# Kernel optimization log

Measured on AMD Instinct MI355X. Metric: run time of the kernel, lower is better.

The kernel has to match this reference:

```python
import jax, jax.numpy as jnp
import numpy as np

EMBED_DIM = 256
H = 80
W = 80
N_HEADS = 8
N_POINTS = 4
B = 8


def sine_pe(C, h, w):
    # LoFTR-style PositionEncodingSine, returns [1, C, h, w]
    y_pos = jnp.cumsum(jnp.ones((h, w), jnp.float32), axis=0)[None]
    x_pos = jnp.cumsum(jnp.ones((h, w), jnp.float32), axis=1)[None]
    div = jnp.exp(jnp.arange(0, C // 2, 2, dtype=jnp.float32) * (-np.log(10000.0) / (C // 2)))[:, None, None]
    pe = jnp.zeros((C, h, w), jnp.float32)
    pe = pe.at[0::4].set(jnp.sin(x_pos * div))
    pe = pe.at[1::4].set(jnp.cos(x_pos * div))
    pe = pe.at[2::4].set(jnp.sin(y_pos * div))
    pe = pe.at[3::4].set(jnp.cos(y_pos * div))
    return pe[None]


def make_reference_points(h, w):
    # Faithful to the original (W-major flatten, (col, row) stacking)
    gr = np.linspace(0, 1, w)
    gc = np.linspace(0, 1, h)
    R, Cg = np.meshgrid(gr, gc, indexing='ij')  # (w, h)
    ref = np.stack((Cg, R), -1).reshape(-1, 2)  # [w*h, 2]
    return jnp.asarray(ref, jnp.float32)


def setup_inputs():
    key = jax.random.key(0)
    ks = jax.random.split(key, 8)
    C = EMBED_DIM
    s = 1.0 / np.sqrt(C)
    return {
        'query': jax.random.normal(ks[0], (B, C, H, W), jnp.float32),
        'value': jax.random.normal(ks[1], (B, C, H, W), jnp.float32),
        'W_value': jax.random.normal(ks[2], (C, C), jnp.float32) * s,
        'b_value': jnp.zeros((C,), jnp.float32),
        'W_off': jax.random.normal(ks[3], (C, N_HEADS * N_POINTS * 2), jnp.float32) * 0.01,
        'b_off': jax.random.normal(ks[4], (N_HEADS * N_POINTS * 2,), jnp.float32) * 0.5,
        'W_attn': jax.random.normal(ks[5], (C, N_HEADS * N_POINTS), jnp.float32) * s,
        'b_attn': jnp.zeros((N_HEADS * N_POINTS,), jnp.float32),
        'W_out': jax.random.normal(ks[6], (C, C), jnp.float32) * s,
        'b_out': jnp.zeros((C,), jnp.float32),
    }


def _deform_attn_core(q, v, ref, W_off, b_off, W_attn, b_attn):
    # q: [B, Nq, C] queries; v: [B, H*W, C] projected values; ref: [Nq, 2]
    Bq, Nq, C = q.shape
    hd = C // N_HEADS
    off = (q @ W_off + b_off).reshape(Bq, Nq, N_HEADS, N_POINTS, 2)
    aw = jax.nn.softmax((q @ W_attn + b_attn).reshape(Bq, Nq, N_HEADS, N_POINTS), axis=-1)
    norm = jnp.array([W, H], jnp.float32)  # offset normalizer (W, H), num_levels=1
    loc = ref[None, :, None, None, :] + off / norm  # [B, Nq, Hn, P, 2], normalized (x, y)
    loc = loc.transpose(0, 2, 1, 3, 4)  # [B, Hn, Nq, P, 2]
    # grid_sample(align_corners=False, padding_mode='zeros'): pixel = loc*size - 0.5
    x = loc[..., 0] * W - 0.5
    y = loc[..., 1] * H - 0.5
    x0f = jnp.floor(x); y0f = jnp.floor(y)
    wx = x - x0f; wy = y - y0f
    x0 = x0f.astype(jnp.int32); y0 = y0f.astype(jnp.int32)
    vh = v.reshape(Bq, H * W, N_HEADS, hd).transpose(0, 2, 1, 3)  # [B, Hn, HW, hd]

    def gather(ix, iy):
        valid = (ix >= 0) & (ix < W) & (iy >= 0) & (iy < H)
        idx = jnp.clip(iy, 0, H - 1) * W + jnp.clip(ix, 0, W - 1)  # [B, Hn, Nq, P]
        g = jnp.take_along_axis(vh, idx.reshape(Bq, N_HEADS, -1, 1), axis=2)
        return g.reshape(Bq, N_HEADS, Nq, N_POINTS, hd) * valid[..., None].astype(v.dtype)

    samp = (gather(x0, y0) * ((1 - wx) * (1 - wy))[..., None]
            + gather(x0 + 1, y0) * (wx * (1 - wy))[..., None]
            + gather(x0, y0 + 1) * ((1 - wx) * wy)[..., None]
            + gather(x0 + 1, y0 + 1) * (wx * wy)[..., None])  # [B, Hn, Nq, P, hd]
    out = jnp.einsum('bhqpd,bhqp->bqhd', samp, aw.transpose(0, 2, 1, 3))
    return out.reshape(Bq, Nq, C)


def reference(query, value, W_value, b_value, W_off, b_off, W_attn, b_attn, W_out, b_out):
    pe = sine_pe(EMBED_DIM, H, W)
    q = query + pe
    qf = q.reshape(B, EMBED_DIM, H * W).transpose(0, 2, 1)      # [B, Nq, C]
    vf = value.reshape(B, EMBED_DIM, H * W).transpose(0, 2, 1)  # [B, Nv, C]
    vproj = vf @ W_value + b_value
    ref = make_reference_points(H, W)
    attn = _deform_attn_core(qf, vproj, ref, W_off, b_off, W_attn, b_attn)
    attn = attn @ W_out + b_out
    attn = attn + qf  # mmcv MSDeformAttn residual (dropout identity at eval)
    out_img = attn.transpose(0, 2, 1).reshape(B, EMBED_DIM, H, W)
    # nn.Upsample(size=(H, W), bilinear) on an (H, W) map is identity (need_downsample=False)
    return (out_img + value, out_img)
```

## Files before the change

kernel.cpp:

```cpp
#include <hip/hip_runtime.h>
#include <hip/hip_bf16.h>
#include <stdint.h>

#define HH 80
#define WW 80
#define NQ 6400
#define CD 256
#define BB 8
#define OUT_HALF 13107200
#define PE_NEG 0.0719557841560639f

typedef __attribute__((ext_vector_type(4))) float f32x4;
typedef __bf16 bf16_t;
typedef __attribute__((ext_vector_type(8))) __bf16 bf16x8;

using gp1_t = const __attribute__((address_space(1))) void*;
using lp3_t = __attribute__((address_space(3))) void*;

__device__ __forceinline__ void gload_lds16(const void* g, void* l) {
    __builtin_amdgcn_global_load_lds((gp1_t)g, (lp3_t)l, 16, 0, 0);
}

__global__ __launch_bounds__(256) void wprep_kernel(const float* __restrict__ Wv,
                                                    const float* __restrict__ Woff,
                                                    const float* __restrict__ Wattn,
                                                    const float* __restrict__ Wout,
                                                    bf16_t* __restrict__ WvT,
                                                    bf16_t* __restrict__ WoaT,
                                                    bf16_t* __restrict__ WoT) {
    int idx = blockIdx.x * 256 + threadIdx.x;
    if (idx < 65536) {
        int cp = idx >> 8, c = idx & 255;
        WvT[idx] = (bf16_t)Wv[c * 256 + cp];
        WoT[idx] = (bf16_t)Wout[c * 256 + cp];
    }
    if (idx < 96 * 256) {
        int j = idx >> 8, c = idx & 255;
        WoaT[idx] = (bf16_t)(j < 64 ? Woff[c * 64 + j] : Wattn[c * 32 + (j - 64)]);
    }
}

__global__ __launch_bounds__(256, 3) void gemm_vproj(const float* __restrict__ V,
                                                     const bf16_t* __restrict__ Y,
                                                     const float* __restrict__ bias,
                                                     bf16_t* __restrict__ D) {
    __shared__ __align__(16) bf16_t lx[128 * 72];
    __shared__ __align__(16) bf16_t ly[128 * 64];
    int b = blockIdx.x & 7;
    int nloc = (blockIdx.x >> 3) * 128;
    int m0 = b * NQ + nloc;
    int c0 = blockIdx.y * 128;
    const float* src = V + (size_t)b * CD * NQ + nloc;
    int tid = threadIdx.x, wv = tid >> 6, ln = tid & 63;
    f32x4 acc[4][4] = {};
    int wr = (wv >> 1) * 64, wc = (wv & 1) * 64;
    int nl = tid & 31;
    for (int kt = 0; kt < 4; ++kt) {
#pragma unroll
        for (int q8 = 0; q8 < 4; ++q8) {
            int q = wv * 4 + q8;
            int row = q * 8 + (ln >> 3);
            int jj = (ln & 7) ^ (row & 7);
            gload_lds16((const char*)Y + ((size_t)(c0 + row)) * 512 + (size_t)kt * 128 + jj * 16,
                        (char*)ly + q * 1024);
        }
#pragma unroll
        for (int i = 0; i < 4; ++i) {
            int kp = (tid >> 5) + i * 8;
            int k = kp * 2;
            const float* s0 = src + (size_t)(kt * 64 + k) * NQ;
#pragma unroll
            for (int l = 0; l < 4; ++l) {
                int n = nl + 32 * l;
                float v0 = s0[n];
                float v1 = s0[NQ + n];
                union { bf16_t h[2]; uint32_t u; } pk;
                pk.h[0] = (bf16_t)v0; pk.h[1] = (bf16_t)v1;
                *(uint32_t*)((char*)lx + n * 144 + k * 2) = pk.u;
            }
        }
        __syncthreads();
#pragma unroll
        for (int ks = 0; ks < 2; ++ks) {
            bf16x8 xa[4], yb[4];
#pragma unroll
            for (int i = 0; i < 4; i++) {
                int m = wr + i * 16 + (ln & 15);
                xa[i] = *(const bf16x8*)((const char*)lx + m * 144 + ks * 64 + (ln >> 4) * 16);
                int n = wc + i * 16 + (ln & 15);
                int cn = (ks * 4 + (ln >> 4)) ^ (n & 7);
                yb[i] = *(const bf16x8*)((const char*)ly + n * 128 + cn * 16);
            }
#pragma unroll
            for (int i = 0; i < 4; i++)
#pragma unroll
                for (int j = 0; j < 4; j++)
                    acc[i][j] = __builtin_amdgcn_mfma_f32_16x16x32_bf16(xa[i], yb[j], acc[i][j], 0, 0, 0);
        }
        __syncthreads();
    }
#pragma unroll
    for (int i = 0; i < 4; i++)
#pragma unroll
        for (int j = 0; j < 4; j++) {
            int col = c0 + wc + j * 16 + (ln & 15);
            float bv = bias[col];
#pragma unroll
            for (int rg = 0; rg < 4; rg++) {
                int row = m0 + wr + i * 16 + (ln >> 4) * 4 + rg;
                D[(size_t)row * 256 + col] = (bf16_t)(acc[i][j][rg] + bv);
            }
        }
}

__global__ __launch_bounds__(512, 4) void oa_sample_out(
        const float* __restrict__ Q,
        const bf16_t* __restrict__ Woa,
        const float* __restrict__ boff,
        const float* __restrict__ battn,
        const bf16_t* __restrict__ vp,
        const bf16_t* __restrict__ WoT,
        const float* __restrict__ bout,
        const float* __restrict__ value,
        float* __restrict__ out) {
    __shared__ __align__(16) char smem[54272];
    char* sampL = smem;
    bf16_t* lx = (bf16_t*)(smem + 32768);
    bf16_t* ly = (bf16_t*)(smem + 41984);
    bf16_t* oaT = (bf16_t*)(smem + 32768);
    bf16_t* wx = (bf16_t*)(smem + 32768);
    float* tile = (float*)(smem + 32768);

    int bid = blockIdx.x;
    int b = bid & 7;
    int nloc = (bid >> 3) * 64;
    int tid = threadIdx.x, wv = tid >> 6, ln = tid & 63;
    const float* src = Q + (size_t)b * CD * NQ + nloc;

    f32x4 accA[3] = {};
    for (int kt = 0; kt < 4; ++kt) {
        {
            int q = wv;
            int row = q * 8 + (ln >> 3);
            int jj = (ln & 7) ^ (row & 7);
            gload_lds16((const char*)Woa + ((size_t)row) * 512 + (size_t)kt * 128 + jj * 16,
                        (char*)ly + q * 1024);
            if (wv < 4) {
                int q2 = 8 + wv;
                int row2 = q2 * 8 + (ln >> 3);
                int jj2 = (ln & 7) ^ (row2 & 7);
                gload_lds16((const char*)Woa + ((size_t)row2) * 512 + (size_t)kt * 128 + jj2 * 16,
                            (char*)ly + q2 * 1024);
            }
        }
        {
            int n = tid & 63;
            int p = nloc + n;
            int hh = p / WW, ww = p - hh * WW;
#pragma unroll
            for (int i = 0; i < 4; ++i) {
                int kp = (tid >> 6) + i * 8;
                int k = kp * 2;
                int c = kt * 64 + k;
                float d = __expf((float)(2 * (c >> 2)) * -PE_NEG);
                const float* s0 = src + (size_t)c * NQ;
                float pos = (c & 2) ? (float)(hh + 1) : (float)(ww + 1);
                float sv, cv;
                __sincosf(pos * d, &sv, &cv);
                float v0 = s0[n] + sv;
                float v1 = s0[NQ + n] + cv;
                union { bf16_t h2[2]; uint32_t u; } pk;
                pk.h2[0] = (bf16_t)v0; pk.h2[1] = (bf16_t)v1;
                *(uint32_t*)((char*)lx + n * 144 + k * 2) = pk.u;
            }
        }
        __syncthreads();
#pragma unroll
        for (int ks = 0; ks < 2; ++ks) {
            bf16x8 xa, yb[3];
            int m = (wv >> 1) * 16 + (ln & 15);
            xa = *(const bf16x8*)((const char*)lx + m * 144 + ks * 64 + (ln >> 4) * 16);
#pragma unroll
            for (int j = 0; j < 3; j++) {
                int n = ((wv & 1) * 3 + j) * 16 + (ln & 15);
                int cn = (ks * 4 + (ln >> 4)) ^ (n & 7);
                yb[j] = *(const bf16x8*)((const char*)ly + n * 128 + cn * 16);
            }
#pragma unroll
            for (int j = 0; j < 3; j++)
                accA[j] = __builtin_amdgcn_mfma_f32_16x16x32_bf16(xa, yb[j], accA[j], 0, 0, 0);
        }
        __syncthreads();
    }
#pragma unroll
    for (int j = 0; j < 3; j++) {
        int col = ((wv & 1) * 3 + j) * 16 + (ln & 15);
        float bv = col < 64 ? boff[col] : battn[col - 64];
#pragma unroll
        for (int rg = 0; rg < 4; rg++) {
            int rloc = (wv >> 1) * 16 + (ln >> 4) * 4 + rg;
            oaT[rloc * 100 + col] = (bf16_t)(accA[j][rg] + bv);
        }
    }
    __syncthreads();

    {
        int h = (tid >> 1) & 7, sh = tid & 1;
        const bf16_t* vb = vp + (size_t)b * NQ * CD + h * 32 + sh * 16;
#pragma unroll
        for (int rnd = 0; rnd < 2; ++rnd) {
            int q = rnd * 32 + (tid >> 4);
            int n = nloc + q;
            const bf16_t* sq = oaT + q * 100;
            float l0 = (float)sq[64 + h * 4 + 0], l1 = (float)sq[64 + h * 4 + 1];
            float l2 = (float)sq[64 + h * 4 + 2], l3 = (float)sq[64 + h * 4 + 3];
            float mx = fmaxf(fmaxf(l0, l1), fmaxf(l2, l3));
            float e0 = __expf(l0 - mx), e1 = __expf(l1 - mx), e2 = __expf(l2 - mx), e3 = __expf(l3 - mx);
            float inv = 1.f / (e0 + e1 + e2 + e3);
            float aw[4] = {e0 * inv, e1 * inv, e2 * inv, e3 * inv};
            float xb = (float)(n % WW) * (80.f / 79.f) - 0.5f;
            float yb = (float)(n / WW) * (80.f / 79.f) - 0.5f;
            float wgt[16];
            int idx[16];
#pragma unroll
            for (int p = 0; p < 4; p++) {
                float x = xb + (float)sq[h * 8 + p * 2];
                float y = yb + (float)sq[h * 8 + p * 2 + 1];
                float x0f = floorf(x), y0f = floorf(y);
                float wx_ = x - x0f, wy_ = y - y0f;
                int ix = (int)x0f, iy = (int)y0f;
                bool vx0 = (unsigned)ix < (unsigned)WW, vx1 = (unsigned)(ix + 1) < (unsigned)WW;
                bool vy0 = (unsigned)iy < (unsigned)HH, vy1 = (unsigned)(iy + 1) < (unsigned)HH;
                int cx0 = min(max(ix, 0), WW - 1), cx1 = min(max(ix + 1, 0), WW - 1);
                int cy0 = min(max(iy, 0), HH - 1), cy1 = min(max(iy + 1, 0), HH - 1);
                float ap = aw[p];
                wgt[p * 4 + 0] = (vx0 && vy0) ? ap * (1.f - wx_) * (1.f - wy_) : 0.f;
                wgt[p * 4 + 1] = (vx1 && vy0) ? ap * wx_ * (1.f - wy_) : 0.f;
                wgt[p * 4 + 2] = (vx0 && vy1) ? ap * (1.f - wx_) * wy_ : 0.f;
                wgt[p * 4 + 3] = (vx1 && vy1) ? ap * wx_ * wy_ : 0.f;
                idx[p * 4 + 0] = cy0 * WW + cx0;
                idx[p * 4 + 1] = cy0 * WW + cx1;
                idx[p * 4 + 2] = cy1 * WW + cx0;
                idx[p * 4 + 3] = cy1 * WW + cx1;
            }
            float fac[16];
#pragma unroll
            for (int j = 0; j < 16; j++) fac[j] = 0.f;
#pragma unroll
            for (int pc = 0; pc < 16; ++pc) {
                const bf16x8* p8 = (const bf16x8*)(vb + (size_t)idx[pc] * CD);
                bf16x8 v0 = p8[0], v1 = p8[1];
                float w = wgt[pc];
#pragma unroll
                for (int j = 0; j < 8; j++) fac[j] += (float)v0[j] * w;
#pragma unroll
                for (int j = 0; j < 8; j++) fac[8 + j] += (float)v1[j] * w;
            }
            bf16x8 o0, o1;
#pragma unroll
            for (int j = 0; j < 8; j++) { o0[j] = (bf16_t)fac[j]; o1[j] = (bf16_t)fac[8 + j]; }
            int c0 = 4 * h + 2 * sh;
            *(bf16x8*)(sampL + q * 512 + ((c0 ^ (q & 7)) * 16)) = o0;
            *(bf16x8*)(sampL + q * 512 + (((c0 + 1) ^ (q & 7)) * 16)) = o1;
        }
    }
    __syncthreads();

    const float* qp = Q + (size_t)b * CD * NQ;
    const float* vvp = value + (size_t)b * CD * NQ;
    float* o0p = out + (size_t)b * CD * NQ;
    float* o1p = out + OUT_HALF + (size_t)b * CD * NQ;
    int mg = wv >> 1, nh = wv & 1;
    for (int p = 0; p < 2; ++p) {
        int cb = p * 128;
        f32x4 acc[2][2] = {};
        for (int kt = 0; kt < 4; ++kt) {
#pragma unroll
            for (int q8 = 0; q8 < 2; ++q8) {
                int q = wv * 2 + q8;
                int row = q * 8 + (ln >> 3);
                int jj = (ln & 7) ^ (row & 7);
                gload_lds16((const char*)WoT + ((size_t)(cb + row)) * 512 + (size_t)kt * 128 + jj * 16,
                            (char*)wx + q * 1024);
            }
            __syncthreads();
#pragma unroll
            for (int ks = 0; ks < 2; ++ks) {
                bf16x8 xa[2], yb[2];
#pragma unroll
                for (int i = 0; i < 2; i++) {
                    int m = mg * 32 + i * 16 + (ln & 15);
                    int ch = (ks * 4 + (ln >> 4)) ^ (m & 7);
                    xa[i] = *(const bf16x8*)((const char*)wx + m * 128 + ch * 16);
                }
#pragma unroll
                for (int j = 0; j < 2; j++) {
                    int nr = nh * 32 + j * 16 + (ln & 15);
                    int cj = kt * 8 + ks * 4 + (ln >> 4);
                    yb[j] = *(const bf16x8*)(sampL + nr * 512 + ((cj ^ (nr & 7)) * 16));
                }
#pragma unroll
                for (int i = 0; i < 2; i++)
#pragma unroll
                    for (int j = 0; j < 2; j++)
                        acc[i][j] = __builtin_amdgcn_mfma_f32_16x16x32_bf16(xa[i], yb[j], acc[i][j], 0, 0, 0);
            }
            __syncthreads();
        }
#pragma unroll
        for (int hp = 0; hp < 2; ++hp) {
            if ((wv >> 2) == hp) {
#pragma unroll
                for (int i = 0; i < 2; i++)
#pragma unroll
                    for (int j = 0; j < 2; j++) {
                        int c = nh * 32 + j * 16 + (ln & 15);
#pragma unroll
                        for (int rg = 0; rg < 4; rg++) {
                            int r = (mg & 1) * 32 + i * 16 + (ln >> 4) * 4 + rg;
                            tile[r * 68 + c] = acc[i][j][rg] + bout[cb + hp * 64 + r];
                        }
                    }
            }
            __syncthreads();
            int g4 = (tid & 15) * 4;
            int rowbase = tid >> 4;
#pragma unroll
            for (int jj = 0; jj < 2; ++jj) {
                int r = rowbase + jj * 32;
                int crow = cb + hp * 64 + r;
                size_t off = (size_t)crow * NQ + nloc + g4;
                f32x4 tv = *(const f32x4*)&tile[r * 68 + g4];
                f32x4 qv = *(const f32x4*)(qp + off);
                f32x4 vv = *(const f32x4*)(vvp + off);
                float d = __expf((float)(2 * (crow >> 2)) * -PE_NEG);
                bool useY = (crow & 2) != 0, odd = (crow & 1) != 0;
                f32x4 pv;
#pragma unroll
                for (int e = 0; e < 4; ++e) {
                    int n = nloc + g4 + e;
                    int hh = n / WW, ww = n - hh * WW;
                    float pos = useY ? (float)(hh + 1) : (float)(ww + 1);
                    float sv, cv;
                    __sincosf(pos * d, &sv, &cv);
                    pv[e] = odd ? cv : sv;
                }
                f32x4 o1v = tv + qv + pv;
                *(f32x4*)(o1p + off) = o1v;
                *(f32x4*)(o0p + off) = o1v + vv;
            }
            __syncthreads();
        }
    }
}

extern "C" void kernel_launch(void* const* d_in, const int* in_sizes, int n_in,
                              void* d_out, int out_size, void* d_ws, size_t ws_size,
                              hipStream_t stream) {
    const float* query   = (const float*)d_in[0];
    const float* value   = (const float*)d_in[1];
    const float* W_value = (const float*)d_in[2];
    const float* b_value = (const float*)d_in[3];
    const float* W_off   = (const float*)d_in[4];
    const float* b_off   = (const float*)d_in[5];
    const float* W_attn  = (const float*)d_in[6];
    const float* b_attn  = (const float*)d_in[7];
    const float* W_out   = (const float*)d_in[8];
    const float* b_out   = (const float*)d_in[9];
    float* out = (float*)d_out;
    char* ws = (char*)d_ws;

    bf16_t* WvT   = (bf16_t*)(ws + 0);
    bf16_t* WoT   = (bf16_t*)(ws + 131072);
    bf16_t* WoaT  = (bf16_t*)(ws + 262144);
    bf16_t* vprojB= (bf16_t*)(ws + 311296);

    wprep_kernel<<<256, 256, 0, stream>>>(W_value, W_off, W_attn, W_out, WvT, WoaT, WoT);
    gemm_vproj<<<dim3(400, 2), 256, 0, stream>>>(value, WvT, b_value, vprojB);
    oa_sample_out<<<800, 512, 0, stream>>>(query, WoaT, b_off, b_attn, vprojB,
                                           WoT, b_out, value, out);
}
```

Measured before the change: 109.7 us.

## Halve query tile per block in fused sample/output kernel to raise occupancy

The fused offset/attention, sampling and output-projection kernel now handles 32 queries per block with 256 threads instead of 64 queries with 512 threads, and launches 1600 blocks. Shared memory drops from about 53KB to 32KB by aliasing the input staging buffers onto the sample buffer region. Wave-to-tile mappings for both MFMA GEMMs and the epilogue are reworked to fit. More resident blocks and better tail balance are the goal, at the cost of loading the weight tiles (Woa, WoT) twice as often per query.

```diff
diff --git a/kernel.cpp b/kernel.cpp
--- a/kernel.cpp
+++ b/kernel.cpp
@@ -113,7 +113,7 @@
         }
 }
 
-__global__ __launch_bounds__(512, 4) void oa_sample_out(
+__global__ __launch_bounds__(256, 5) void oa_sample_out(
         const float* __restrict__ Q,
         const bf16_t* __restrict__ Woa,
         const float* __restrict__ boff,
@@ -123,43 +123,38 @@
         const float* __restrict__ bout,
         const float* __restrict__ value,
         float* __restrict__ out) {
-    __shared__ __align__(16) char smem[54272];
+    __shared__ __align__(16) char smem[32768];
     char* sampL = smem;
-    bf16_t* lx = (bf16_t*)(smem + 32768);
-    bf16_t* ly = (bf16_t*)(smem + 41984);
-    bf16_t* oaT = (bf16_t*)(smem + 32768);
-    bf16_t* wx = (bf16_t*)(smem + 32768);
-    float* tile = (float*)(smem + 32768);
+    bf16_t* lx = (bf16_t*)smem;
+    bf16_t* ly = (bf16_t*)(smem + 16384);
+    bf16_t* oaT = (bf16_t*)(smem + 16384);
+    bf16_t* wx = (bf16_t*)(smem + 16384);
+    float* tile = (float*)(smem + 16384);
 
     int bid = blockIdx.x;
     int b = bid & 7;
-    int nloc = (bid >> 3) * 64;
+    int nloc = (bid >> 3) * 32;
     int tid = threadIdx.x, wv = tid >> 6, ln = tid & 63;
     const float* src = Q + (size_t)b * CD * NQ + nloc;
 
     f32x4 accA[3] = {};
+    int mi = wv & 1, nh3 = wv >> 1;
     for (int kt = 0; kt < 4; ++kt) {
-        {
-            int q = wv;
+#pragma unroll
+        for (int q3 = 0; q3 < 3; ++q3) {
+            int q = wv * 3 + q3;
             int row = q * 8 + (ln >> 3);
             int jj = (ln & 7) ^ (row & 7);
             gload_lds16((const char*)Woa + ((size_t)row) * 512 + (size_t)kt * 128 + jj * 16,
                         (char*)ly + q * 1024);
-            if (wv < 4) {
-                int q2 = 8 + wv;
-                int row2 = q2 * 8 + (ln >> 3);
-                int jj2 = (ln & 7) ^ (row2 & 7);
-                gload_lds16((const char*)Woa + ((size_t)row2) * 512 + (size_t)kt * 128 + jj2 * 16,
-                            (char*)ly + q2 * 1024);
-            }
         }
         {
-            int n = tid & 63;
+            int n = tid & 31;
             int p = nloc + n;
             int hh = p / WW, ww = p - hh * WW;
 #pragma unroll
             for (int i = 0; i < 4; ++i) {
-                int kp = (tid >> 6) + i * 8;
+                int kp = (tid >> 5) + i * 8;
                 int k = kp * 2;
                 int c = kt * 64 + k;
                 float d = __expf((float)(2 * (c >> 2)) * -PE_NEG);
@@ -178,11 +173,11 @@
 #pragma unroll
         for (int ks = 0; ks < 2; ++ks) {
             bf16x8 xa, yb[3];
-            int m = (wv >> 1) * 16 + (ln & 15);
+            int m = mi * 16 + (ln & 15);
             xa = *(const bf16x8*)((const char*)lx + m * 144 + ks * 64 + (ln >> 4) * 16);
 #pragma unroll
             for (int j = 0; j < 3; j++) {
-                int n = ((wv & 1) * 3 + j) * 16 + (ln & 15);
+                int n = (nh3 * 3 + j) * 16 + (ln & 15);
                 int cn = (ks * 4 + (ln >> 4)) ^ (n & 7);
                 yb[j] = *(const bf16x8*)((const char*)ly + n * 128 + cn * 16);
             }
@@ -194,11 +189,11 @@
     }
 #pragma unroll
     for (int j = 0; j < 3; j++) {
-        int col = ((wv & 1) * 3 + j) * 16 + (ln & 15);
+        int col = (nh3 * 3 + j) * 16 + (ln & 15);
         float bv = col < 64 ? boff[col] : battn[col - 64];
 #pragma unroll
         for (int rg = 0; rg < 4; rg++) {
-            int rloc = (wv >> 1) * 16 + (ln >> 4) * 4 + rg;
+            int rloc = mi * 16 + (ln >> 4) * 4 + rg;
             oaT[rloc * 100 + col] = (bf16_t)(accA[j][rg] + bv);
         }
     }
@@ -209,7 +204,7 @@
         const bf16_t* vb = vp + (size_t)b * NQ * CD + h * 32 + sh * 16;
 #pragma unroll
         for (int rnd = 0; rnd < 2; ++rnd) {
-            int q = rnd * 32 + (tid >> 4);
+            int q = rnd * 16 + (tid >> 4);
             int n = nloc + q;
             const bf16_t* sq = oaT + q * 100;
             float l0 = (float)sq[64 + h * 4 + 0], l1 = (float)sq[64 + h * 4 + 1];
@@ -273,11 +268,13 @@
     int mg = wv >> 1, nh = wv & 1;
     for (int p = 0; p < 2; ++p) {
         int cb = p * 128;
-        f32x4 acc[2][2] = {};
+        f32x4 acc[4];
+#pragma unroll
+        for (int i = 0; i < 4; i++) acc[i] = (f32x4){0.f, 0.f, 0.f, 0.f};
         for (int kt = 0; kt < 4; ++kt) {
 #pragma unroll
-            for (int q8 = 0; q8 < 2; ++q8) {
-                int q = wv * 2 + q8;
+            for (int q8 = 0; q8 < 4; ++q8) {
+                int q = wv * 4 + q8;
                 int row = q * 8 + (ln >> 3);
                 int jj = (ln & 7) ^ (row & 7);
                 gload_lds16((const char*)WoT + ((size_t)(cb + row)) * 512 + (size_t)kt * 128 + jj * 16,
@@ -286,51 +283,46 @@
             __syncthreads();
 #pragma unroll
             for (int ks = 0; ks < 2; ++ks) {
-                bf16x8 xa[2], yb[2];
-#pragma unroll
-                for (int i = 0; i < 2; i++) {
-                    int m = mg * 32 + i * 16 + (ln & 15);
+                bf16x8 xa[4], yb;
+#pragma unroll
+                for (int i = 0; i < 4; i++) {
+                    int m = mg * 64 + i * 16 + (ln & 15);
                     int ch = (ks * 4 + (ln >> 4)) ^ (m & 7);
                     xa[i] = *(const bf16x8*)((const char*)wx + m * 128 + ch * 16);
                 }
-#pragma unroll
-                for (int j = 0; j < 2; j++) {
-                    int nr = nh * 32 + j * 16 + (ln & 15);
+                {
+                    int nr = nh * 16 + (ln & 15);
                     int cj = kt * 8 + ks * 4 + (ln >> 4);
-                    yb[j] = *(const bf16x8*)(sampL + nr * 512 + ((cj ^ (nr & 7)) * 16));
+                    yb = *(const bf16x8*)(sampL + nr * 512 + ((cj ^ (nr & 7)) * 16));
                 }
 #pragma unroll
-                for (int i = 0; i < 2; i++)
-#pragma unroll
-                    for (int j = 0; j < 2; j++)
-                        acc[i][j] = __builtin_amdgcn_mfma_f32_16x16x32_bf16(xa[i], yb[j], acc[i][j], 0, 0, 0);
+                for (int i = 0; i < 4; i++)
+                    acc[i] = __builtin_amdgcn_mfma_f32_16x16x32_bf16(xa[i], yb, acc[i], 0, 0, 0);
             }
             __syncthreads();
         }
 #pragma unroll
         for (int hp = 0; hp < 2; ++hp) {
-            if ((wv >> 2) == hp) {
-#pragma unroll
-                for (int i = 0; i < 2; i++)
-#pragma unroll
-                    for (int j = 0; j < 2; j++) {
-                        int c = nh * 32 + j * 16 + (ln & 15);
-#pragma unroll
-                        for (int rg = 0; rg < 4; rg++) {
-                            int r = (mg & 1) * 32 + i * 16 + (ln >> 4) * 4 + rg;
-                            tile[r * 68 + c] = acc[i][j][rg] + bout[cb + hp * 64 + r];
-                        }
+            if (mg == hp) {
+#pragma unroll
+                for (int i = 0; i < 4; i++) {
+                    int c = nh * 16 + (ln & 15);
+#pragma unroll
+                    for (int rg = 0; rg < 4; rg++) {
+                        int r = i * 16 + (ln >> 4) * 4 + rg;
+                        tile[r * 36 + c] = acc[i][rg] + bout[cb + hp * 64 + r];
                     }
+                }
             }
             __syncthreads();
-            int g4 = (tid & 15) * 4;
-            int rowbase = tid >> 4;
+            int g4 = (tid & 7) * 4;
+            int rowbase = tid >> 3;
 #pragma unroll
             for (int jj = 0; jj < 2; ++jj) {
                 int r = rowbase + jj * 32;
                 int crow = cb + hp * 64 + r;
                 size_t off = (size_t)crow * NQ + nloc + g4;
-                f32x4 tv = *(const f32x4*)&tile[r * 68 + g4];
+                f32x4 tv = *(const f32x4*)&tile[r * 36 + g4];
                 f32x4 qv = *(const f32x4*)(qp + off);
                 f32x4 vv = *(const f32x4*)(vvp + off);
                 float d = __expf((float)(2 * (crow >> 2)) * -PE_NEG);
@@ -377,6 +369,6 @@
 
     wprep_kernel<<<256, 256, 0, stream>>>(W_value, W_off, W_attn, W_out, WvT, WoaT, WoT);
     gemm_vproj<<<dim3(400, 2), 256, 0, stream>>>(value, WvT, b_value, vprojB);
-    oa_sample_out<<<800, 512, 0, stream>>>(query, WoaT, b_off, b_attn, vprojB,
-                                           WoT, b_out, value, out);
-}
+    oa_sample_out<<<1600, 256, 0, stream>>>(query, WoaT, b_off, b_attn, vprojB,
+                                            WoT, b_out, value, out);
+}
```

After: 205.3 us. +87.1%, slower.
